# Kernel tuning notes

Hardware: AMD Instinct MI355X
Metric: run time of the kernel (lower is better)

## Reference

```python
import jax, jax.numpy as jnp
import numpy as np

N = 100000   # nodes
E = 3200000  # directed edges
F_IN = 128   # data.num_node_features
H = 16       # hidden
C = 2        # output classes (hard-coded in module)


def _glorot(key, fan_in, fan_out):
    s = jnp.sqrt(6.0 / (fan_in + fan_out)).astype(jnp.float32)
    return jax.random.uniform(key, (fan_in, fan_out), jnp.float32, -s, s)


def setup_inputs() -> dict:
    key = jax.random.key(0)
    ks = jax.random.split(key, 5)
    x = jax.random.normal(ks[0], (N, F_IN), jnp.float32)
    edge_index = jax.random.randint(ks[1], (2, E), 0, N, dtype=jnp.int64)
    return {
        "x": x,
        "edge_index": edge_index,
        "W1": _glorot(ks[2], F_IN, H), "b1": jnp.zeros((H,), jnp.float32),
        "W2": _glorot(ks[3], H, H),    "b2": jnp.zeros((H,), jnp.float32),
        "W3": _glorot(ks[4], H, C),    "b3": jnp.zeros((C,), jnp.float32),
    }


def _gcn_conv(x, W, b, src, dst, norm, n):
    # PyG GCNConv: linear transform, then normalized gather -> scatter-add, + bias
    h = x @ W                                   # [N, out]
    msg = h[src] * norm[:, None]                # [E+N, out] gather over source nodes
    out = jax.ops.segment_sum(msg, dst, num_segments=n)  # scatter-add at targets
    return out + b


def reference(x, edge_index, W1, b1, W2, b2, W3, b3):
    n = x.shape[0]
    loop = jnp.arange(n, dtype=edge_index.dtype)
    src = jnp.concatenate([edge_index[0], loop])  # add self-loops (PyG default)
    dst = jnp.concatenate([edge_index[1], loop])
    # symmetric normalization: deg^{-1/2}[src] * deg^{-1/2}[dst], deg = in-degree w/ self-loops
    deg = jax.ops.segment_sum(jnp.ones(src.shape, jnp.float32), dst, num_segments=n)
    dis = jnp.where(deg > 0, jax.lax.rsqrt(jnp.maximum(deg, 1.0)), 0.0)
    norm = dis[src] * dis[dst]
    # dropout is identity in eval mode
    h = jax.nn.relu(_gcn_conv(x, W1, b1, src, dst, norm, n))
    h = jax.nn.relu(_gcn_conv(h, W2, b2, src, dst, norm, n))
    h = _gcn_conv(h, W3, b3, src, dst, norm, n)
    return jax.nn.log_softmax(h, axis=1)
```

## Files before the change

kernel.cpp:

```cpp
#include <hip/hip_runtime.h>
#include <math.h>

#define NSB   512
#define BSH   8
#define BKN   256
#define ESMAX 6272

typedef _Float16 h8  __attribute__((ext_vector_type(8)));
typedef _Float16 h4  __attribute__((ext_vector_type(4)));
typedef _Float16 h2v __attribute__((ext_vector_type(2)));


__global__ void k_scan1(const int* __restrict__ in, int* __restrict__ out,
                        int* __restrict__ bsum, int n) {
    __shared__ int sd[256];
    int base = blockIdx.x * 2048 + threadIdx.x * 8;
    int v[8];
    int ts = 0;
#pragma unroll
    for (int j = 0; j < 8; j++) {
        int idx = base + j;
        v[j] = ts;
        ts += (idx < n) ? in[idx] : 0;
    }
    sd[threadIdx.x] = ts;
    __syncthreads();
    for (int ofs = 1; ofs < 256; ofs <<= 1) {
        int t = (threadIdx.x >= (unsigned)ofs) ? sd[threadIdx.x - ofs] : 0;
        __syncthreads();
        sd[threadIdx.x] += t;
        __syncthreads();
    }
    int excl = (threadIdx.x == 0) ? 0 : sd[threadIdx.x - 1];
#pragma unroll
    for (int j = 0; j < 8; j++) {
        int idx = base + j;
        if (idx < n) out[idx] = excl + v[j];
    }
    if (threadIdx.x == 255) bsum[blockIdx.x] = sd[255];
}

__global__ void k_scan2(int* __restrict__ bsum, int nb) {
    __shared__ int sd[256];
    int orig = (threadIdx.x < (unsigned)nb) ? bsum[threadIdx.x] : 0;
    sd[threadIdx.x] = orig;
    __syncthreads();
    for (int ofs = 1; ofs < 256; ofs <<= 1) {
        int t = (threadIdx.x >= (unsigned)ofs) ? sd[threadIdx.x - ofs] : 0;
        __syncthreads();
        sd[threadIdx.x] += t;
        __syncthreads();
    }
    if (threadIdx.x < (unsigned)nb) bsum[threadIdx.x] = sd[threadIdx.x] - orig;
}


__global__ void k_hist(const int* __restrict__ dst, int* __restrict__ hist,
                       int e, int nbuck, int es) {
    __shared__ int h[512];
    for (int i = threadIdx.x; i < 512; i += blockDim.x) h[i] = 0;
    __syncthreads();
    int lo = blockIdx.x * es;
    int hi = min(lo + es, e);
    for (int i = lo + threadIdx.x; i < hi; i += blockDim.x)
        atomicAdd(&h[dst[i] >> BSH], 1);
    __syncthreads();
    for (int i = threadIdx.x; i < nbuck; i += blockDim.x)
        hist[(size_t)i * gridDim.x + blockIdx.x] = h[i];
}

__global__ void k_bucket(const int* __restrict__ src, const int* __restrict__ dst,
                         const int* __restrict__ hist, const int* __restrict__ offs,
                         const int* __restrict__ bsum, unsigned* __restrict__ col,
                         int e, int nbuck, int es) {
    __shared__ unsigned sorted[ESMAX];
    __shared__ unsigned char sbuck[ESMAX];
    __shared__ int lc[512], lsc[512], lofE[512], lcur[512], soff[512];
    int tid = threadIdx.x;
    if (tid < nbuck) {
        size_t idx = (size_t)tid * gridDim.x + blockIdx.x;
        lc[tid] = hist[idx];
        soff[tid] = offs[idx] + bsum[idx >> 11];
    } else {
        lc[tid] = 0;
    }
    __syncthreads();
    int lo = blockIdx.x * es;
    int hi = min(lo + es, e);
    lsc[tid] = lc[tid];
    __syncthreads();
    for (int ofs = 1; ofs < 512; ofs <<= 1) {
        int t = (tid >= ofs) ? lsc[tid - ofs] : 0;
        __syncthreads();
        lsc[tid] += t;
        __syncthreads();
    }
    int excl = (tid == 0) ? 0 : lsc[tid - 1];
    lofE[tid] = excl;
    lcur[tid] = excl;
    __syncthreads();
    for (int i = lo + tid; i < hi; i += 512) {
        int d = dst[i];
        int b = d >> BSH;
        int p = atomicAdd(&lcur[b], 1);
        sorted[p] = ((unsigned)src[i] << BSH) | (unsigned)(d & (BKN - 1));
        sbuck[p] = (unsigned char)(b & 255);
    }
    __syncthreads();
    int cnt_ = hi - lo;
    int split = (nbuck > 256) ? lofE[256] : 0x7fffffff;
    for (int i = tid; i < cnt_; i += 512) {
        int b = sbuck[i] | ((i >= split) ? 256 : 0);
        col[soff[b] + (i - lofE[b])] = sorted[i];
    }
}

__global__ void k_sort(const unsigned* __restrict__ col, const int* __restrict__ offs,
                       const int* __restrict__ bsum, int* __restrict__ col2,
                       int* __restrict__ rs, float* __restrict__ dis,
                       int n, int e, int nbuck) {
    __shared__ int cnt[BKN];
    __shared__ int sd[BKN];
    __shared__ int cur[BKN];
    int tid = threadIdx.x;
    int b = blockIdx.x;
    size_t i0 = (size_t)b * NSB;
    int lo = offs[i0] + bsum[i0 >> 11];
    int hi = e;
    if (b + 1 < nbuck) {
        size_t i1 = (size_t)(b + 1) * NSB;
        hi = offs[i1] + bsum[i1 >> 11];
    }
    if (tid < BKN) cnt[tid] = 0;
    __syncthreads();
    for (int i = lo + tid; i < hi; i += 512)
        atomicAdd(&cnt[col[i] & (BKN - 1u)], 1);
    __syncthreads();
    if (tid < BKN) sd[tid] = cnt[tid];
    __syncthreads();
    for (int ofs = 1; ofs < BKN; ofs <<= 1) {
        int t = (tid < BKN && tid >= ofs) ? sd[tid - ofs] : 0;
        __syncthreads();
        if (tid < BKN) sd[tid] += t;
        __syncthreads();
    }
    if (tid < BKN) {
        int excl = (tid == 0) ? 0 : sd[tid - 1];
        cur[tid] = lo + excl;
        int node = (b << BSH) + tid;
        if (node < n) {
            rs[node] = lo + excl;
            dis[node] = rsqrtf((float)(cnt[tid] + 1));
        }
    }
    if (b == 0 && tid == 0) rs[n] = e;
    __syncthreads();
    for (int i = lo + tid; i < hi; i += 512) {
        unsigned v = col[i];
        int pos = atomicAdd(&cur[v & (BKN - 1u)], 1);
        col2[pos] = (int)(v >> BSH);
    }
}


__global__ __launch_bounds__(512) void k_linear1s(
        const float* __restrict__ x, const float* __restrict__ W,
        const float* __restrict__ dis, _Float16* __restrict__ hs, int n) {
    __shared__ float sW[2048];
    int tid = threadIdx.x;
    for (int i = tid; i < 2048; i += 512) sW[i] = W[i];
    __syncthreads();
    int cg = tid & 3;
    int kg = (tid >> 2) & 7;
    int nl = tid >> 5;
    float wr[16][4];
#pragma unroll
    for (int j = 0; j < 16; j++)
#pragma unroll
        for (int cc = 0; cc < 4; cc++)
            wr[j][cc] = sW[(kg * 16 + j) * 16 + cg * 4 + cc];
    int nodeBase = blockIdx.x * 128 + nl;
    for (int it = 0; it < 8; it++) {
        int node = nodeBase + it * 16;
        float a0 = 0.f, a1 = 0.f, a2 = 0.f, a3 = 0.f;
        if (node < n) {
            const float4* xr = (const float4*)(x + (size_t)node * 128 + kg * 16);
#pragma unroll
            for (int j4 = 0; j4 < 4; j4++) {
                float4 xv = xr[j4];
                float xs0 = xv.x, xs1 = xv.y, xs2 = xv.z, xs3 = xv.w;
                int j = j4 * 4;
                a0 += xs0 * wr[j][0] + xs1 * wr[j+1][0] + xs2 * wr[j+2][0] + xs3 * wr[j+3][0];
                a1 += xs0 * wr[j][1] + xs1 * wr[j+1][1] + xs2 * wr[j+2][1] + xs3 * wr[j+3][1];
                a2 += xs0 * wr[j][2] + xs1 * wr[j+1][2] + xs2 * wr[j+2][2] + xs3 * wr[j+3][2];
                a3 += xs0 * wr[j][3] + xs1 * wr[j+1][3] + xs2 * wr[j+2][3] + xs3 * wr[j+3][3];
            }
        }
#pragma unroll
        for (int m = 4; m <= 16; m <<= 1) {
            a0 += __shfl_xor(a0, m);
            a1 += __shfl_xor(a1, m);
            a2 += __shfl_xor(a2, m);
            a3 += __shfl_xor(a3, m);
        }
        if (kg == 0 && node < n) {
            float d = dis[node];
            h4 o;
            o[0] = (_Float16)(a0 * d);
            o[1] = (_Float16)(a1 * d);
            o[2] = (_Float16)(a2 * d);
            o[3] = (_Float16)(a3 * d);
            *((h4*)(hs + (size_t)node * 16 + cg * 4)) = o;
        }
    }
}


__global__ void k_pullA(const _Float16* __restrict__ hs, const int* __restrict__ rs,
                        const int* __restrict__ col2, const float* __restrict__ dis,
                        const float* __restrict__ bb, const float* __restrict__ W,
                        _Float16* __restrict__ hsOut, int n) {
    __shared__ float sW[256];
    __shared__ float sb[16];
    if (threadIdx.x < 256) sW[threadIdx.x] = W[threadIdx.x];
    if (threadIdx.x < 16) sb[threadIdx.x] = bb[threadIdx.x];
    __syncthreads();
    int t = blockIdx.x * blockDim.x + threadIdx.x;
    int node = t >> 2, sub = t & 3;
    int q = sub & 1, half = sub >> 1;
    if (node >= n) return;
    const h8* H = (const h8*)hs;
    float acc[8];
    if (half == 0) {
        h8 self = H[(size_t)node * 2 + q];
#pragma unroll
        for (int j = 0; j < 8; j++) acc[j] = (float)self[j];
    } else {
#pragma unroll
        for (int j = 0; j < 8; j++) acc[j] = 0.f;
    }
    int b = rs[node], e2 = rs[node + 1];
    int mid = b + ((e2 - b) >> 1);
    int i  = half ? mid : b;
    int en = half ? e2  : mid;
    for (; i + 3 < en; i += 4) {
        int s0 = col2[i], s1 = col2[i + 1], s2 = col2[i + 2], s3 = col2[i + 3];
        h8 v0 = H[(size_t)s0 * 2 + q];
        h8 v1 = H[(size_t)s1 * 2 + q];
        h8 v2 = H[(size_t)s2 * 2 + q];
        h8 v3 = H[(size_t)s3 * 2 + q];
#pragma unroll
        for (int j = 0; j < 8; j++)
            acc[j] += (float)v0[j] + (float)v1[j] + (float)v2[j] + (float)v3[j];
    }
    for (; i < en; i++) {
        h8 v = H[(size_t)col2[i] * 2 + q];
#pragma unroll
        for (int j = 0; j < 8; j++) acc[j] += (float)v[j];
    }
#pragma unroll
    for (int j = 0; j < 8; j++) acc[j] += __shfl_xor(acc[j], 2);
    float d = dis[node];
    float va[16];
#pragma unroll
    for (int j = 0; j < 8; j++) {
        int k = q * 8 + j;
        float v = acc[j] * d + sb[k];
        v = v > 0.f ? v : 0.f;
        float other = __shfl_xor(v, 1);
        va[j]     = q ? other : v;
        va[8 + j] = q ? v : other;
    }
    if (half == 0) {
        h8 o;
#pragma unroll
        for (int j = 0; j < 8; j++) {
            int c = q * 8 + j;
            float s = 0.f;
#pragma unroll
            for (int k = 0; k < 16; k++) s += va[k] * sW[k * 16 + c];
            o[j] = (_Float16)(s * d);
        }
        ((h8*)hsOut)[(size_t)node * 2 + q] = o;
    }
}


__global__ void k_pullB(const _Float16* __restrict__ hs, const int* __restrict__ rs,
                        const int* __restrict__ col2, const float* __restrict__ dis,
                        const float* __restrict__ bb, const float* __restrict__ W,
                        _Float16* __restrict__ hs2, int n) {
    __shared__ float sW[32];
    __shared__ float sb[16];
    if (threadIdx.x < 32) sW[threadIdx.x] = W[threadIdx.x];
    if (threadIdx.x < 16) sb[threadIdx.x] = bb[threadIdx.x];
    __syncthreads();
    int t = blockIdx.x * blockDim.x + threadIdx.x;
    int node = t >> 2, sub = t & 3;
    int q = sub & 1, half = sub >> 1;
    if (node >= n) return;
    const h8* H = (const h8*)hs;
    float acc[8];
    if (half == 0) {
        h8 self = H[(size_t)node * 2 + q];
#pragma unroll
        for (int j = 0; j < 8; j++) acc[j] = (float)self[j];
    } else {
#pragma unroll
        for (int j = 0; j < 8; j++) acc[j] = 0.f;
    }
    int b = rs[node], e2 = rs[node + 1];
    int mid = b + ((e2 - b) >> 1);
    int i  = half ? mid : b;
    int en = half ? e2  : mid;
    for (; i + 3 < en; i += 4) {
        int s0 = col2[i], s1 = col2[i + 1], s2 = col2[i + 2], s3 = col2[i + 3];
        h8 v0 = H[(size_t)s0 * 2 + q];
        h8 v1 = H[(size_t)s1 * 2 + q];
        h8 v2 = H[(size_t)s2 * 2 + q];
        h8 v3 = H[(size_t)s3 * 2 + q];
#pragma unroll
        for (int j = 0; j < 8; j++)
            acc[j] += (float)v0[j] + (float)v1[j] + (float)v2[j] + (float)v3[j];
    }
    for (; i < en; i++) {
        h8 v = H[(size_t)col2[i] * 2 + q];
#pragma unroll
        for (int j = 0; j < 8; j++) acc[j] += (float)v[j];
    }
#pragma unroll
    for (int j = 0; j < 8; j++) acc[j] += __shfl_xor(acc[j], 2);
    float d = dis[node];
    float p0 = 0.f, p1 = 0.f;
#pragma unroll
    for (int j = 0; j < 8; j++) {
        int k = q * 8 + j;
        float v = acc[j] * d + sb[k];
        v = v > 0.f ? v : 0.f;
        p0 += v * sW[k * 2 + 0];
        p1 += v * sW[k * 2 + 1];
    }
    p0 += __shfl_xor(p0, 1);
    p1 += __shfl_xor(p1, 1);
    if (sub == 0) {
        h2v o;
        o[0] = (_Float16)(p0 * d);
        o[1] = (_Float16)(p1 * d);
        ((h2v*)hs2)[node] = o;
    }
}


__global__ void k_pull2lsm(const _Float16* __restrict__ hs2, const int* __restrict__ rs,
                           const int* __restrict__ col2, const float* __restrict__ dis,
                           const float* __restrict__ b3, float* __restrict__ out, int n) {
    int t = blockIdx.x * blockDim.x + threadIdx.x;
    int node = t >> 1, half = t & 1;
    if (node >= n) return;
    const h2v* H = (const h2v*)hs2;
    float a0 = 0.f, a1 = 0.f;
    if (half == 0) {
        h2v self = H[node];
        a0 = (float)self[0]; a1 = (float)self[1];
    }
    int b = rs[node], e2 = rs[node + 1];
    int mid = b + ((e2 - b) >> 1);
    int i  = half ? mid : b;
    int en = half ? e2  : mid;
    for (; i + 3 < en; i += 4) {
        h2v v0 = H[col2[i]];
        h2v v1 = H[col2[i + 1]];
        h2v v2 = H[col2[i + 2]];
        h2v v3 = H[col2[i + 3]];
        a0 += (float)v0[0] + (float)v1[0] + (float)v2[0] + (float)v3[0];
        a1 += (float)v0[1] + (float)v1[1] + (float)v2[1] + (float)v3[1];
    }
    for (; i < en; i++) {
        h2v v = H[col2[i]];
        a0 += (float)v[0];
        a1 += (float)v[1];
    }
    a0 += __shfl_xor(a0, 1);
    a1 += __shfl_xor(a1, 1);
    if (half == 0) {
        float d = dis[node];
        float z0 = a0 * d + b3[0];
        float z1 = a1 * d + b3[1];
        float m = fmaxf(z0, z1);
        float l = m + logf(expf(z0 - m) + expf(z1 - m));
        float2 o = {z0 - l, z1 - l};
        ((float2*)out)[node] = o;
    }
}


extern "C" void kernel_launch(void* const* d_in, const int* in_sizes, int n_in,
                              void* d_out, int out_size, void* d_ws, size_t ws_size,
                              hipStream_t stream) {
    const float* x  = (const float*)d_in[0];
    const int*   ei = (const int*)d_in[1];
    const float* W1 = (const float*)d_in[2];
    const float* b1 = (const float*)d_in[3];
    const float* W2 = (const float*)d_in[4];
    const float* b2 = (const float*)d_in[5];
    const float* W3 = (const float*)d_in[6];
    const float* b3 = (const float*)d_in[7];
    float* out = (float*)d_out;

    const int N = in_sizes[0] / 128;
    const int E = in_sizes[1] / 2;
    const int* src = ei;
    const int* dst = ei + E;

    const int NBUCK = (N + BKN - 1) >> BSH;
    const int M = NBUCK * NSB;
    const int ES = (E + NSB - 1) / NSB;

    char* ws = (char*)d_ws;
    size_t off = 0;
    auto alloc = [&](size_t bytes) {
        void* p = ws + off;
        off += (bytes + 255) & ~(size_t)255;
        return p;
    };
    int*       hist = (int*)alloc((size_t)M * sizeof(int));
    int*       offs = (int*)alloc((size_t)M * sizeof(int));
    int*       bsum = (int*)alloc(256 * sizeof(int));
    unsigned*  col  = (unsigned*)alloc((size_t)E * sizeof(unsigned));
    int*       col2 = (int*)alloc((size_t)E * sizeof(int));
    int*       rs   = (int*)alloc((size_t)(N + 1) * sizeof(int));
    float*     dis  = (float*)alloc((size_t)N * sizeof(float));
    _Float16*  hsA  = (_Float16*)alloc((size_t)N * 16 * sizeof(_Float16));
    _Float16*  hsB  = (_Float16*)alloc((size_t)N * 16 * sizeof(_Float16));
    _Float16*  hs2  = (_Float16*)alloc((size_t)N * 2 * sizeof(_Float16));

    const int B = 256;
    auto g = [&](long long work) { return (int)((work + B - 1) / B); };
    const int NBS = (M + 2047) / 2048;

    k_hist<<<NSB, B, 0, stream>>>(dst, hist, E, NBUCK, ES);
    k_scan1<<<NBS, 256, 0, stream>>>(hist, offs, bsum, M);
    k_scan2<<<1, 256, 0, stream>>>(bsum, NBS);
    k_bucket<<<NSB, 512, 0, stream>>>(src, dst, hist, offs, bsum, col, E, NBUCK, ES);
    k_sort<<<NBUCK, 512, 0, stream>>>(col, offs, bsum, col2, rs, dis, N, E, NBUCK);

    k_linear1s<<<(N + 127) / 128, 512, 0, stream>>>(x, W1, dis, hsA, N);

    k_pullA<<<g((long long)N * 4), B, 0, stream>>>(hsA, rs, col2, dis, b1, W2, hsB, N);

    k_pullB<<<g((long long)N * 4), B, 0, stream>>>(hsB, rs, col2, dis, b2, W3, hs2, N);

    k_pull2lsm<<<g((long long)N * 2), B, 0, stream>>>(hs2, rs, col2, dis, b3, out, N);
}
```

Baseline: 259.5 us.

## Use wave-shuffle scans and split pull aggregation across four edge ranges

Replaces the shared-memory Hillis-Steele scans in the scan, bucket and sort kernels with 64-lane shuffle scans plus a small per-wave sum combine, removing many barriers. The three pull kernels now split each node's edge list four ways instead of two, doubling threads per node, and reduce the partial sums with an extra xor shuffle. This adds parallelism to the latency-bound gather loops (about 32 edges per node) at the cost of more threads, more shuffles and shorter per-thread loops that often fall back to the scalar tail.

```diff
diff --git a/kernel.cpp b/kernel.cpp
--- a/kernel.cpp
+++ b/kernel.cpp
@@ -10,10 +10,20 @@
 typedef _Float16 h4  __attribute__((ext_vector_type(4)));
 typedef _Float16 h2v __attribute__((ext_vector_type(2)));
 
+__device__ inline int wave_scan_incl(int v) {
+    int lane = threadIdx.x & 63;
+#pragma unroll
+    for (int d = 1; d < 64; d <<= 1) {
+        int t = __shfl_up(v, d, 64);
+        if (lane >= d) v += t;
+    }
+    return v;
+}
+
 
 __global__ void k_scan1(const int* __restrict__ in, int* __restrict__ out,
                         int* __restrict__ bsum, int n) {
-    __shared__ int sd[256];
+    __shared__ int wsum[4];
     int base = blockIdx.x * 2048 + threadIdx.x * 8;
     int v[8];
     int ts = 0;
@@ -23,35 +33,33 @@
         v[j] = ts;
         ts += (idx < n) ? in[idx] : 0;
     }
-    sd[threadIdx.x] = ts;
-    __syncthreads();
-    for (int ofs = 1; ofs < 256; ofs <<= 1) {
-        int t = (threadIdx.x >= (unsigned)ofs) ? sd[threadIdx.x - ofs] : 0;
-        __syncthreads();
-        sd[threadIdx.x] += t;
-        __syncthreads();
-    }
-    int excl = (threadIdx.x == 0) ? 0 : sd[threadIdx.x - 1];
+    int inc = wave_scan_incl(ts);
+    int wid = threadIdx.x >> 6;
+    if ((threadIdx.x & 63) == 63) wsum[wid] = inc;
+    __syncthreads();
+    int wofs = 0;
+#pragma unroll
+    for (int w = 0; w < 4; w++) wofs += (w < wid) ? wsum[w] : 0;
+    int excl = inc - ts + wofs;
 #pragma unroll
     for (int j = 0; j < 8; j++) {
         int idx = base + j;
         if (idx < n) out[idx] = excl + v[j];
     }
-    if (threadIdx.x == 255) bsum[blockIdx.x] = sd[255];
+    if (threadIdx.x == 255) bsum[blockIdx.x] = excl + ts;
 }
 
 __global__ void k_scan2(int* __restrict__ bsum, int nb) {
-    __shared__ int sd[256];
+    __shared__ int wsum[4];
     int orig = (threadIdx.x < (unsigned)nb) ? bsum[threadIdx.x] : 0;
-    sd[threadIdx.x] = orig;
-    __syncthreads();
-    for (int ofs = 1; ofs < 256; ofs <<= 1) {
-        int t = (threadIdx.x >= (unsigned)ofs) ? sd[threadIdx.x - ofs] : 0;
-        __syncthreads();
-        sd[threadIdx.x] += t;
-        __syncthreads();
-    }
-    if (threadIdx.x < (unsigned)nb) bsum[threadIdx.x] = sd[threadIdx.x] - orig;
+    int inc = wave_scan_incl(orig);
+    int wid = threadIdx.x >> 6;
+    if ((threadIdx.x & 63) == 63) wsum[wid] = inc;
+    __syncthreads();
+    int wofs = 0;
+#pragma unroll
+    for (int w = 0; w < 4; w++) wofs += (w < wid) ? wsum[w] : 0;
+    if (threadIdx.x < (unsigned)nb) bsum[threadIdx.x] = inc - orig + wofs;
 }
 
 
@@ -75,30 +83,28 @@
                          int e, int nbuck, int es) {
     __shared__ unsigned sorted[ESMAX];
     __shared__ unsigned char sbuck[ESMAX];
-    __shared__ int lc[512], lsc[512], lofE[512], lcur[512], soff[512];
+    __shared__ int lofE[512], lcur[512], soff[512];
+    __shared__ int wsum[8];
     int tid = threadIdx.x;
+    int lc = 0;
     if (tid < nbuck) {
         size_t idx = (size_t)tid * gridDim.x + blockIdx.x;
-        lc[tid] = hist[idx];
+        lc = hist[idx];
         soff[tid] = offs[idx] + bsum[idx >> 11];
-    } else {
-        lc[tid] = 0;
-    }
+    }
+    int inc = wave_scan_incl(lc);
+    int wid = tid >> 6;
+    if ((tid & 63) == 63) wsum[wid] = inc;
+    __syncthreads();
+    int wofs = 0;
+#pragma unroll
+    for (int w = 0; w < 8; w++) wofs += (w < wid) ? wsum[w] : 0;
+    int excl = inc - lc + wofs;
+    lofE[tid] = excl;
+    lcur[tid] = excl;
     __syncthreads();
     int lo = blockIdx.x * es;
     int hi = min(lo + es, e);
-    lsc[tid] = lc[tid];
-    __syncthreads();
-    for (int ofs = 1; ofs < 512; ofs <<= 1) {
-        int t = (tid >= ofs) ? lsc[tid - ofs] : 0;
-        __syncthreads();
-        lsc[tid] += t;
-        __syncthreads();
-    }
-    int excl = (tid == 0) ? 0 : lsc[tid - 1];
-    lofE[tid] = excl;
-    lcur[tid] = excl;
-    __syncthreads();
     for (int i = lo + tid; i < hi; i += 512) {
         int d = dst[i];
         int b = d >> BSH;
@@ -120,8 +126,8 @@
                        int* __restrict__ rs, float* __restrict__ dis,
                        int n, int e, int nbuck) {
     __shared__ int cnt[BKN];
-    __shared__ int sd[BKN];
     __shared__ int cur[BKN];
+    __shared__ int wsum[4];
     int tid = threadIdx.x;
     int b = blockIdx.x;
     size_t i0 = (size_t)b * NSB;
@@ -136,21 +142,21 @@
     for (int i = lo + tid; i < hi; i += 512)
         atomicAdd(&cnt[col[i] & (BKN - 1u)], 1);
     __syncthreads();
-    if (tid < BKN) sd[tid] = cnt[tid];
-    __syncthreads();
-    for (int ofs = 1; ofs < BKN; ofs <<= 1) {
-        int t = (tid < BKN && tid >= ofs) ? sd[tid - ofs] : 0;
-        __syncthreads();
-        if (tid < BKN) sd[tid] += t;
-        __syncthreads();
-    }
+    int c = (tid < BKN) ? cnt[tid] : 0;
+    int inc = wave_scan_incl(c);
+    int wid = tid >> 6;
+    if (tid < BKN && (tid & 63) == 63) wsum[wid] = inc;
+    __syncthreads();
     if (tid < BKN) {
-        int excl = (tid == 0) ? 0 : sd[tid - 1];
+        int wofs = 0;
+#pragma unroll
+        for (int w = 0; w < 4; w++) wofs += (w < wid) ? wsum[w] : 0;
+        int excl = inc - c + wofs;
         cur[tid] = lo + excl;
         int node = (b << BSH) + tid;
         if (node < n) {
             rs[node] = lo + excl;
-            dis[node] = rsqrtf((float)(cnt[tid] + 1));
+            dis[node] = rsqrtf((float)(c + 1));
         }
     }
     if (b == 0 && tid == 0) rs[n] = e;
@@ -225,13 +231,13 @@
     if (threadIdx.x < 256) sW[threadIdx.x] = W[threadIdx.x];
     if (threadIdx.x < 16) sb[threadIdx.x] = bb[threadIdx.x];
     __syncthreads();
-    int t = blockIdx.x * blockDim.x + threadIdx.x;
-    int node = t >> 2, sub = t & 3;
-    int q = sub & 1, half = sub >> 1;
+    long long t = (long long)blockIdx.x * blockDim.x + threadIdx.x;
+    int node = (int)(t >> 3), sub = (int)(t & 7);
+    int q = sub & 1, qt = sub >> 1;
     if (node >= n) return;
     const h8* H = (const h8*)hs;
     float acc[8];
-    if (half == 0) {
+    if (qt == 0) {
         h8 self = H[(size_t)node * 2 + q];
 #pragma unroll
         for (int j = 0; j < 8; j++) acc[j] = (float)self[j];
@@ -240,9 +246,9 @@
         for (int j = 0; j < 8; j++) acc[j] = 0.f;
     }
     int b = rs[node], e2 = rs[node + 1];
-    int mid = b + ((e2 - b) >> 1);
-    int i  = half ? mid : b;
-    int en = half ? e2  : mid;
+    int len = e2 - b;
+    int i  = b + ((len * qt) >> 2);
+    int en = b + ((len * (qt + 1)) >> 2);
     for (; i + 3 < en; i += 4) {
         int s0 = col2[i], s1 = col2[i + 1], s2 = col2[i + 2], s3 = col2[i + 3];
         h8 v0 = H[(size_t)s0 * 2 + q];
@@ -259,7 +265,10 @@
         for (int j = 0; j < 8; j++) acc[j] += (float)v[j];
     }
 #pragma unroll
-    for (int j = 0; j < 8; j++) acc[j] += __shfl_xor(acc[j], 2);
+    for (int j = 0; j < 8; j++) {
+        acc[j] += __shfl_xor(acc[j], 2);
+        acc[j] += __shfl_xor(acc[j], 4);
+    }
     float d = dis[node];
     float va[16];
 #pragma unroll
@@ -271,7 +280,7 @@
         va[j]     = q ? other : v;
         va[8 + j] = q ? v : other;
     }
-    if (half == 0) {
+    if (qt == 0) {
         h8 o;
 #pragma unroll
         for (int j = 0; j < 8; j++) {
@@ -295,13 +304,13 @@
     if (threadIdx.x < 32) sW[threadIdx.x] = W[threadIdx.x];
     if (threadIdx.x < 16) sb[threadIdx.x] = bb[threadIdx.x];
     __syncthreads();
-    int t = blockIdx.x * blockDim.x + threadIdx.x;
-    int node = t >> 2, sub = t & 3;
-    int q = sub & 1, half = sub >> 1;
+    long long t = (long long)blockIdx.x * blockDim.x + threadIdx.x;
+    int node = (int)(t >> 3), sub = (int)(t & 7);
+    int q = sub & 1, qt = sub >> 1;
     if (node >= n) return;
     const h8* H = (const h8*)hs;
     float acc[8];
-    if (half == 0) {
+    if (qt == 0) {
         h8 self = H[(size_t)node * 2 + q];
 #pragma unroll
         for (int j = 0; j < 8; j++) acc[j] = (float)self[j];
@@ -310,9 +319,9 @@
         for (int j = 0; j < 8; j++) acc[j] = 0.f;
     }
     int b = rs[node], e2 = rs[node + 1];
-    int mid = b + ((e2 - b) >> 1);
-    int i  = half ? mid : b;
-    int en = half ? e2  : mid;
+    int len = e2 - b;
+    int i  = b + ((len * qt) >> 2);
+    int en = b + ((len * (qt + 1)) >> 2);
     for (; i + 3 < en; i += 4) {
         int s0 = col2[i], s1 = col2[i + 1], s2 = col2[i + 2], s3 = col2[i + 3];
         h8 v0 = H[(size_t)s0 * 2 + q];
@@ -329,7 +338,10 @@
         for (int j = 0; j < 8; j++) acc[j] += (float)v[j];
     }
 #pragma unroll
-    for (int j = 0; j < 8; j++) acc[j] += __shfl_xor(acc[j], 2);
+    for (int j = 0; j < 8; j++) {
+        acc[j] += __shfl_xor(acc[j], 2);
+        acc[j] += __shfl_xor(acc[j], 4);
+    }
     float d = dis[node];
     float p0 = 0.f, p1 = 0.f;
 #pragma unroll
@@ -354,19 +366,19 @@
 __global__ void k_pull2lsm(const _Float16* __restrict__ hs2, const int* __restrict__ rs,
                            const int* __restrict__ col2, const float* __restrict__ dis,
                            const float* __restrict__ b3, float* __restrict__ out, int n) {
-    int t = blockIdx.x * blockDim.x + threadIdx.x;
-    int node = t >> 1, half = t & 1;
+    long long t = (long long)blockIdx.x * blockDim.x + threadIdx.x;
+    int node = (int)(t >> 2), qt = (int)(t & 3);
     if (node >= n) return;
     const h2v* H = (const h2v*)hs2;
     float a0 = 0.f, a1 = 0.f;
-    if (half == 0) {
+    if (qt == 0) {
         h2v self = H[node];
         a0 = (float)self[0]; a1 = (float)self[1];
     }
     int b = rs[node], e2 = rs[node + 1];
-    int mid = b + ((e2 - b) >> 1);
-    int i  = half ? mid : b;
-    int en = half ? e2  : mid;
+    int len = e2 - b;
+    int i  = b + ((len * qt) >> 2);
+    int en = b + ((len * (qt + 1)) >> 2);
     for (; i + 3 < en; i += 4) {
         h2v v0 = H[col2[i]];
         h2v v1 = H[col2[i + 1]];
@@ -380,9 +392,9 @@
         a0 += (float)v[0];
         a1 += (float)v[1];
     }
-    a0 += __shfl_xor(a0, 1);
-    a1 += __shfl_xor(a1, 1);
-    if (half == 0) {
+    a0 += __shfl_xor(a0, 1); a0 += __shfl_xor(a0, 2);
+    a1 += __shfl_xor(a1, 1); a1 += __shfl_xor(a1, 2);
+    if (qt == 0) {
         float d = dis[node];
         float z0 = a0 * d + b3[0];
         float z1 = a1 * d + b3[1];
@@ -446,9 +458,9 @@
 
     k_linear1s<<<(N + 127) / 128, 512, 0, stream>>>(x, W1, dis, hsA, N);
 
-    k_pullA<<<g((long long)N * 4), B, 0, stream>>>(hsA, rs, col2, dis, b1, W2, hsB, N);
-
-    k_pullB<<<g((long long)N * 4), B, 0, stream>>>(hsB, rs, col2, dis, b2, W3, hs2, N);
-
-    k_pull2lsm<<<g((long long)N * 2), B, 0, stream>>>(hs2, rs, col2, dis, b3, out, N);
-}
+    k_pullA<<<g((long long)N * 8), B, 0, stream>>>(hsA, rs, col2, dis, b1, W2, hsB, N);
+
+    k_pullB<<<g((long long)N * 8), B, 0, stream>>>(hsB, rs, col2, dis, b2, W3, hs2, N);
+
+    k_pull2lsm<<<g((long long)N * 4), B, 0, stream>>>(hs2, rs, col2, dis, b3, out, N);
+}
```

Result: faster. 247.8 us (-4.5%).
